# Optimization experiments

Measured on AMD Instinct MI355X. Metric: run time of the kernel, lower is better.

Reference implementation:

```python
import jax, jax.numpy as jnp
import numpy as np

B, S, H = 2, 4096, 1024
WINDOW = 32


def setup_inputs() -> dict:
    key = jax.random.key(0)
    ks = jax.random.split(key, 10)
    s = 1.0 / np.sqrt(H)
    return {
        "hidden_states": jax.random.normal(ks[0], (B, S, H), dtype=jnp.float32),
        "Wq": jax.random.normal(ks[1], (H, H), dtype=jnp.float32) * s,
        "Wk": jax.random.normal(ks[2], (H, H), dtype=jnp.float32) * s,
        "Wv": jax.random.normal(ks[3], (H, H), dtype=jnp.float32) * s,
        "Wo": jax.random.normal(ks[4], (H, H), dtype=jnp.float32) * s,
        "ln_w": jnp.ones((H,), dtype=jnp.float32),
        "ln_b": jnp.zeros((H,), dtype=jnp.float32),
        "W1": jax.random.normal(ks[5], (H // 2, H), dtype=jnp.float32) * s,
        "b1": jnp.zeros((H // 2,), dtype=jnp.float32),
        "W2": jax.random.normal(ks[6], (H, H // 2), dtype=jnp.float32) * (1.0 / np.sqrt(H // 2)),
        "b2": jnp.zeros((H,), dtype=jnp.float32),
    }


def _layernorm(x, w, b, eps=1e-5):
    mu = jnp.mean(x, axis=-1, keepdims=True)
    var = jnp.var(x, axis=-1, keepdims=True)
    return (x - mu) * jax.lax.rsqrt(var + eps) * w + b


def reference(hidden_states, Wq, Wk, Wv, Wo, ln_w, ln_b, W1, b1, W2, b2):
    x = hidden_states  # [B,S,H]
    q = x @ Wq.T
    k = x @ Wk.T
    v = x @ Wv.T
    # banded causal mask: keep j<=i and j >= i-WINDOW+1
    i = jnp.arange(S)[:, None]
    j = jnp.arange(S)[None, :]
    local_mask = (j <= i) & (j >= i - WINDOW + 1)  # [S,S] bool
    scores = jnp.einsum('bqh,bkh->bqk', q, k) / np.sqrt(H)
    scores = jnp.where(local_mask[None], scores, -jnp.inf)
    probs = jax.nn.softmax(scores, axis=-1)
    attn_out = jnp.einsum('bqk,bkh->bqh', probs, v) @ Wo.T
    draft = x + attn_out
    h = _layernorm(draft, ln_w, ln_b)
    h = jax.nn.gelu(h @ W1.T + b1, approximate=False)
    adapter_out = h @ W2.T + b2
    return draft + adapter_out
```

## Files before the change

### kernel.cpp

```cpp
#include <hip/hip_runtime.h>
#include <stdint.h>

typedef unsigned short u16;
typedef __bf16 bfx8 __attribute__((ext_vector_type(8)));
typedef float f32x4 __attribute__((ext_vector_type(4)));

__device__ __forceinline__ u16 f2bf(float x) {
    unsigned int u = __float_as_uint(x);
    u += 0x7fffu + ((u >> 16) & 1u);
    return (u16)(u >> 16);
}

__device__ __forceinline__ void async16(const void* g, void* l) {
    __builtin_amdgcn_global_load_lds(
        (const __attribute__((address_space(1))) unsigned int*)(uintptr_t)g,
        (__attribute__((address_space(3))) unsigned int*)(unsigned int)(uintptr_t)l,
        16, 0, 0);
}

#define S_BARRIER() asm volatile("s_barrier" ::: "memory")
#define WAIT_VM(n) asm volatile("s_waitcnt vmcnt(" #n ")" ::: "memory")

struct CastArgs {
    const float* src[7];
    u16* dst[7];
    int nblk[7];
};
__global__ __launch_bounds__(256) void cast_all(CastArgs a) {
    int b = blockIdx.x, seg = 0;
    while (b >= a.nblk[seg]) { b -= a.nblk[seg]; ++seg; }
    int i = b * 256 + threadIdx.x;
    const float4* p = (const float4*)(a.src[seg] + (size_t)i * 8);
    float4 x = p[0], y = p[1];
    ushort4 o0, o1;
    o0.x = f2bf(x.x); o0.y = f2bf(x.y); o0.z = f2bf(x.z); o0.w = f2bf(x.w);
    o1.x = f2bf(y.x); o1.y = f2bf(y.y); o1.z = f2bf(y.z); o1.w = f2bf(y.w);
    ushort4* q = (ushort4*)(a.dst[seg] + (size_t)i * 8);
    q[0] = o0; q[1] = o1;
}

template <int EPI>
__global__ __launch_bounds__(512, 2)
void gemm_nt(const u16* __restrict__ A, const u16* __restrict__ Bw,
             u16* __restrict__ outb, float* __restrict__ outf,
             const float* __restrict__ res, const float* __restrict__ bias,
             u16* __restrict__ outq, u16* __restrict__ outk,
             u16* __restrict__ vt, int M, int N, int K) {
    __shared__ __align__(1024) unsigned char lds[147456];
    const int t = threadIdx.x;
    const int lane = t & 63, w = t >> 6;
    const int laneR = lane & 15, laneK = lane >> 4;
    const int wr = w >> 1, wc = w & 1;
    const int row0 = blockIdx.y * 256, col0 = blockIdx.x * 128;
    const int nt = K >> 6;

    f32x4 acc[4][4] = {};

    const u16* srcA[4];
    const u16* srcB[2];
    unsigned dA[4], dB[2];
#pragma unroll
    for (int i = 0; i < 4; ++i) {
        int li = i * 512 + t;
        int row = li >> 3, ko = li & 7;
        srcA[i] = A + (size_t)(row0 + row) * K + (ko ^ (row & 7)) * 8;
        dA[i] = li * 16;
    }
#pragma unroll
    for (int i = 0; i < 2; ++i) {
        int li = i * 512 + t;
        int row = li >> 3, ko = li & 7;
        srcB[i] = Bw + (size_t)(col0 + row) * K + (ko ^ (row & 7)) * 8;
        dB[i] = 32768 + li * 16;
    }

    auto stage = [&](int b, int tk, int h) {
        unsigned char* base = lds + b * 49152;
        const int o = tk * 64;
        if (h == 0) {
            async16(srcA[0] + o, base + dA[0]);
            async16(srcA[1] + o, base + dA[1]);
            async16(srcB[0] + o, base + dB[0]);
        } else {
            async16(srcA[2] + o, base + dA[2]);
            async16(srcA[3] + o, base + dA[3]);
            async16(srcB[1] + o, base + dB[1]);
        }
    };

    stage(0, 0, 0); stage(0, 0, 1);
    stage(1, 1, 0); stage(1, 1, 1);

    for (int tk = 0; tk < nt; ++tk) {
        unsigned char* bufA = lds + (tk % 3) * 49152;
        unsigned char* bufB = bufA + 32768;
        if (tk + 1 < nt) { WAIT_VM(6); } else { WAIT_VM(0); }
        S_BARRIER();
        const bool pf = (tk + 2 < nt);
        const int nb = (tk + 2) % 3;
#pragma unroll
        for (int ks = 0; ks < 2; ++ks) {
            bfx8 af[4], bf[4];
#pragma unroll
            for (int m = 0; m < 4; ++m) {
                int r = wr * 64 + m * 16 + laneR;
                int phys = (ks * 4 + laneK) ^ (r & 7);
                af[m] = *(const bfx8*)(bufA + r * 128 + phys * 16);
            }
#pragma unroll
            for (int n = 0; n < 4; ++n) {
                int r = wc * 64 + n * 16 + laneR;
                int phys = (ks * 4 + laneK) ^ (r & 7);
                bf[n] = *(const bfx8*)(bufB + r * 128 + phys * 16);
            }
            if (pf) stage(nb, tk + 2, ks);
            S_BARRIER();
            __builtin_amdgcn_s_setprio(1);
#pragma unroll
            for (int m = 0; m < 4; ++m)
#pragma unroll
                for (int n = 0; n < 4; ++n)
                    acc[m][n] = __builtin_amdgcn_mfma_f32_16x16x32_bf16(
                        af[m], bf[n], acc[m][n], 0, 0, 0);
            __builtin_amdgcn_s_setprio(0);
            S_BARRIER();
        }
    }

#pragma unroll
    for (int m = 0; m < 4; ++m) {
        const int gr0 = row0 + wr * 64 + m * 16 + laneK * 4;
#pragma unroll
        for (int n = 0; n < 4; ++n) {
            const int gc = col0 + wc * 64 + n * 16 + laneR;
            if constexpr (EPI == 0) {
                if (col0 < 1024) {
#pragma unroll
                    for (int r = 0; r < 4; ++r)
                        outq[(size_t)(gr0 + r) * 1024 + gc] = f2bf(acc[m][n][r]);
                } else if (col0 < 2048) {
#pragma unroll
                    for (int r = 0; r < 4; ++r)
                        outk[(size_t)(gr0 + r) * 1024 + (gc - 1024)] = f2bf(acc[m][n][r]);
                } else {
                    ushort4 o4;
                    o4.x = f2bf(acc[m][n][0]); o4.y = f2bf(acc[m][n][1]);
                    o4.z = f2bf(acc[m][n][2]); o4.w = f2bf(acc[m][n][3]);
                    *(ushort4*)(vt + (((size_t)(gr0 >> 12)) * 1024 + (gc - 2048)) * 4096 +
                                (gr0 & 4095)) = o4;
                }
            } else if constexpr (EPI == 1) {
#pragma unroll
                for (int r = 0; r < 4; ++r) {
                    size_t idx = (size_t)(gr0 + r) * N + gc;
                    outf[idx] = res[idx] + acc[m][n][r];
                }
            } else if constexpr (EPI == 2) {
#pragma unroll
                for (int r = 0; r < 4; ++r) {
                    float xx = acc[m][n][r] + bias[gc];
                    outb[(size_t)(gr0 + r) * N + gc] =
                        f2bf(xx * 0.5f * (1.0f + erff(xx * 0.70710678118654752f)));
                }
            } else {
#pragma unroll
                for (int r = 0; r < 4; ++r) {
                    size_t idx = (size_t)(gr0 + r) * N + gc;
                    outf[idx] = res[idx] + acc[m][n][r] + bias[gc];
                }
            }
        }
    }
}

__global__ __launch_bounds__(256, 2)
void attn_kernel(const u16* __restrict__ Q, const u16* __restrict__ K,
                 const u16* __restrict__ vt, u16* __restrict__ O) {
    constexpr int H = 1024, S = 4096;
    const int t = threadIdx.x, lane = t & 63, w = t >> 6;
    const int laneR = lane & 15, laneK = lane >> 4;
    const int tile = blockIdx.x;
    const int batch = tile >> 7;
    const int i0 = (tile & 127) * 32;
    const size_t base = (size_t)batch * S * H;

    __shared__ __align__(16) float S4[4][32][64];
    __shared__ __align__(16) u16 P[32][72];

    f32x4 sc[2][4] = {};
    for (int h = w * 256; h < w * 256 + 256; h += 32) {
        bfx8 qa[2];
#pragma unroll
        for (int m = 0; m < 2; ++m) {
            size_t row = (size_t)(i0 + m * 16 + laneR);
            qa[m] = *(const bfx8*)(Q + base + row * H + h + laneK * 8);
        }
        bfx8 kb[4];
#pragma unroll
        for (int n = 0; n < 4; ++n) {
            int j = i0 - 32 + n * 16 + laneR;
            int jc = j < 0 ? 0 : j;
            kb[n] = *(const bfx8*)(K + base + (size_t)jc * H + h + laneK * 8);
        }
#pragma unroll
        for (int m = 0; m < 2; ++m)
#pragma unroll
            for (int n = 0; n < 4; ++n)
                sc[m][n] = __builtin_amdgcn_mfma_f32_16x16x32_bf16(
                    qa[m], kb[n], sc[m][n], 0, 0, 0);
    }
#pragma unroll
    for (int m = 0; m < 2; ++m)
#pragma unroll
        for (int n = 0; n < 4; ++n)
#pragma unroll
            for (int r = 0; r < 4; ++r)
                S4[w][m * 16 + laneK * 4 + r][n * 16 + laneR] = sc[m][n][r];
    __syncthreads();

    {
        int q = t >> 3;
        int c0 = (t & 7) * 8;
        int lo = q + 1;
        if (32 - i0 > lo) lo = 32 - i0;
        int hi = q + 32;
        float vals[8];
        float mx = -1e30f;
#pragma unroll
        for (int c = 0; c < 8; ++c) {
            int cc = c0 + c;
            float v = (S4[0][q][cc] + S4[1][q][cc] + S4[2][q][cc] + S4[3][q][cc]) * 0.03125f;
            bool valid = (cc >= lo) && (cc <= hi);
            vals[c] = valid ? v : -1e30f;
            if (vals[c] > mx) mx = vals[c];
        }
#pragma unroll
        for (int d = 1; d < 8; d <<= 1) {
            float o = __shfl_xor(mx, d);
            if (o > mx) mx = o;
        }
        float sum = 0.f;
        float es[8];
#pragma unroll
        for (int c = 0; c < 8; ++c) {
            es[c] = (vals[c] > -1e29f) ? __expf(vals[c] - mx) : 0.f;
            sum += es[c];
        }
#pragma unroll
        for (int d = 1; d < 8; d <<= 1) sum += __shfl_xor(sum, d);
        float inv = 1.0f / sum;
#pragma unroll
        for (int c = 0; c < 8; ++c) P[q][c0 + c] = f2bf(es[c] * inv);
    }
    __syncthreads();

    for (int nc = 0; nc < 4; ++nc) {
        int ncol = w * 256 + nc * 64;
        f32x4 o[2][4] = {};
#pragma unroll
        for (int ks = 0; ks < 2; ++ks) {
            bfx8 pa[2];
#pragma unroll
            for (int m = 0; m < 2; ++m)
                pa[m] = *(const bfx8*)(&P[m * 16 + laneR][ks * 32 + laneK * 8]);
            int t0 = i0 - 32 + ks * 32 + laneK * 8;
            if (t0 < 0) t0 = 0;
#pragma unroll
            for (int n = 0; n < 4; ++n) {
                int c = ncol + n * 16 + laneR;
                bfx8 vb = *(const bfx8*)(vt + ((size_t)batch * 1024 + c) * 4096 + t0);
#pragma unroll
                for (int m = 0; m < 2; ++m)
                    o[m][n] = __builtin_amdgcn_mfma_f32_16x16x32_bf16(
                        pa[m], vb, o[m][n], 0, 0, 0);
            }
        }
#pragma unroll
        for (int m = 0; m < 2; ++m)
#pragma unroll
            for (int n = 0; n < 4; ++n)
#pragma unroll
                for (int r = 0; r < 4; ++r) {
                    size_t row = (size_t)(i0 + m * 16 + laneK * 4 + r);
                    O[base + row * H + ncol + n * 16 + laneR] = f2bf(o[m][n][r]);
                }
    }
}

__global__ __launch_bounds__(256)
void ln_kernel(const float* __restrict__ x, const float* __restrict__ gw,
               const float* __restrict__ gb, u16* __restrict__ out) {
    const int row = blockIdx.x, t = threadIdx.x;
    const float4 v = ((const float4*)(x + (size_t)row * 1024))[t];
    float s = v.x + v.y + v.z + v.w;
    float s2 = v.x * v.x + v.y * v.y + v.z * v.z + v.w * v.w;
#pragma unroll
    for (int d = 1; d < 64; d <<= 1) {
        s += __shfl_xor(s, d);
        s2 += __shfl_xor(s2, d);
    }
    __shared__ float red[8];
    int lane = t & 63, wv = t >> 6;
    if (lane == 0) { red[wv] = s; red[4 + wv] = s2; }
    __syncthreads();
    float S1 = red[0] + red[1] + red[2] + red[3];
    float S2 = red[4] + red[5] + red[6] + red[7];
    float mu = S1 * (1.0f / 1024.0f);
    float var = S2 * (1.0f / 1024.0f) - mu * mu;
    float rstd = rsqrtf(var + 1e-5f);
    const float4 wv4 = ((const float4*)gw)[t];
    const float4 bv4 = ((const float4*)gb)[t];
    ushort4 o;
    o.x = f2bf((v.x - mu) * rstd * wv4.x + bv4.x);
    o.y = f2bf((v.y - mu) * rstd * wv4.y + bv4.y);
    o.z = f2bf((v.z - mu) * rstd * wv4.z + bv4.z);
    o.w = f2bf((v.w - mu) * rstd * wv4.w + bv4.w);
    ((ushort4*)(out + (size_t)row * 1024))[t] = o;
}

extern "C" void kernel_launch(void* const* d_in, const int* in_sizes, int n_in,
                              void* d_out, int out_size, void* d_ws, size_t ws_size,
                              hipStream_t stream) {
    const float* x   = (const float*)d_in[0];
    const float* Wq  = (const float*)d_in[1];
    const float* Wk  = (const float*)d_in[2];
    const float* Wv  = (const float*)d_in[3];
    const float* Wo  = (const float*)d_in[4];
    const float* lnw = (const float*)d_in[5];
    const float* lnb = (const float*)d_in[6];
    const float* W1  = (const float*)d_in[7];
    const float* b1  = (const float*)d_in[8];
    const float* W2  = (const float*)d_in[9];
    const float* b2  = (const float*)d_in[10];
    (void)in_sizes; (void)n_in; (void)out_size; (void)ws_size;

    const int M = 8192, H = 1024, Hh = 512;

    char* ws = (char*)d_ws;
    size_t off = 0;
    auto alloc = [&](size_t bytes) {
        char* p = ws + off;
        off += (bytes + 255) & ~(size_t)255;
        return p;
    };
    u16* Xb    = (u16*)alloc((size_t)M * H * 2);
    u16* Wqkvb = (u16*)alloc((size_t)3 * H * H * 2);
    u16* Wob   = (u16*)alloc((size_t)H * H * 2);
    u16* W1b   = (u16*)alloc((size_t)Hh * H * 2);
    u16* W2b   = (u16*)alloc((size_t)H * Hh * 2);
    u16* Qb    = (u16*)alloc((size_t)M * H * 2);
    u16* Kb    = (u16*)alloc((size_t)M * H * 2);
    u16* Vt    = (u16*)alloc((size_t)M * H * 2);
    float* draft = (float*)alloc((size_t)M * H * 4);
    u16* Attb = Xb;
    u16* hlnb = Qb;
    u16* Gb   = Kb;
    float* outp = (float*)d_out;

    CastArgs ca;
    ca.src[0] = x;  ca.dst[0] = Xb;                   ca.nblk[0] = (M * H / 8) / 256;
    ca.src[1] = Wq; ca.dst[1] = Wqkvb;                ca.nblk[1] = (H * H / 8) / 256;
    ca.src[2] = Wk; ca.dst[2] = Wqkvb + (size_t)H * H;     ca.nblk[2] = (H * H / 8) / 256;
    ca.src[3] = Wv; ca.dst[3] = Wqkvb + (size_t)2 * H * H; ca.nblk[3] = (H * H / 8) / 256;
    ca.src[4] = Wo; ca.dst[4] = Wob;                  ca.nblk[4] = (H * H / 8) / 256;
    ca.src[5] = W1; ca.dst[5] = W1b;                  ca.nblk[5] = (Hh * H / 8) / 256;
    ca.src[6] = W2; ca.dst[6] = W2b;                  ca.nblk[6] = (H * Hh / 8) / 256;
    int totblk = 0;
    for (int i = 0; i < 7; ++i) totblk += ca.nblk[i];
    cast_all<<<dim3(totblk), dim3(256), 0, stream>>>(ca);

    dim3 gblk(512);
    gemm_nt<0><<<dim3(3 * H / 128, M / 256), gblk, 0, stream>>>(
        Xb, Wqkvb, nullptr, nullptr, nullptr, nullptr, Qb, Kb, Vt, M, 3 * H, H);

    attn_kernel<<<dim3(256), dim3(256), 0, stream>>>(Qb, Kb, Vt, Attb);

    gemm_nt<1><<<dim3(H / 128, M / 256), gblk, 0, stream>>>(
        Attb, Wob, nullptr, draft, x, nullptr, nullptr, nullptr, nullptr, M, H, H);

    ln_kernel<<<dim3(M), dim3(256), 0, stream>>>(draft, lnw, lnb, hlnb);

    gemm_nt<2><<<dim3(Hh / 128, M / 256), gblk, 0, stream>>>(
        hlnb, W1b, Gb, nullptr, nullptr, b1, nullptr, nullptr, nullptr, M, Hh, H);

    gemm_nt<3><<<dim3(H / 128, M / 256), gblk, 0, stream>>>(
        Gb, W2b, nullptr, outp, draft, b2, nullptr, nullptr, nullptr, M, H, Hh);
}
```

Before: 190.6 us.

## Store draft in bf16, add register-staged GEMM variant, narrow W1 GEMM tiles

The fp32 draft buffer becomes bf16, which halves the traffic for writing draft, reading it in layernorm and reading it again as the residual in the final GEMM. The Wo and W2 GEMMs move to a new kernel that stages global loads through registers into a two-buffer LDS ring instead of using async LDS loads, so each block needs less LDS. The W1 GEMM now uses 64-wide N tiles, giving 256 blocks instead of 128 to fill more CUs. Rounding draft to bf16 adds error to both the residual path and the layernorm input.

```diff
diff --git a/kernel.cpp b/kernel.cpp
--- a/kernel.cpp
+++ b/kernel.cpp
@@ -9,6 +9,9 @@
     unsigned int u = __float_as_uint(x);
     u += 0x7fffu + ((u >> 16) & 1u);
     return (u16)(u >> 16);
+}
+__device__ __forceinline__ float bf2f(u16 v) {
+    return __uint_as_float(((unsigned)v) << 16);
 }
 
 __device__ __forceinline__ void async16(const void* g, void* l) {
@@ -19,7 +22,10 @@
 }
 
 #define S_BARRIER() asm volatile("s_barrier" ::: "memory")
-#define WAIT_VM(n) asm volatile("s_waitcnt vmcnt(" #n ")" ::: "memory")
+#define WAIT_VM6() asm volatile("s_waitcnt vmcnt(6)" ::: "memory")
+#define WAIT_VM5() asm volatile("s_waitcnt vmcnt(5)" ::: "memory")
+#define WAIT_VM0() asm volatile("s_waitcnt vmcnt(0)" ::: "memory")
+#define WAIT_LGKM0() asm volatile("s_waitcnt lgkmcnt(0)" ::: "memory")
 
 struct CastArgs {
     const float* src[7];
@@ -39,26 +45,28 @@
     q[0] = o0; q[1] = o1;
 }
 
-template <int EPI>
+template <int EPI, int BNv>
 __global__ __launch_bounds__(512, 2)
-void gemm_nt(const u16* __restrict__ A, const u16* __restrict__ Bw,
-             u16* __restrict__ outb, float* __restrict__ outf,
-             const float* __restrict__ res, const float* __restrict__ bias,
-             u16* __restrict__ outq, u16* __restrict__ outk,
-             u16* __restrict__ vt, int M, int N, int K) {
-    __shared__ __align__(1024) unsigned char lds[147456];
+void gemm_ring(const u16* __restrict__ A, const u16* __restrict__ Bw,
+               u16* __restrict__ outq, u16* __restrict__ outk,
+               u16* __restrict__ vt, u16* __restrict__ outb,
+               const float* __restrict__ bias, int M, int N, int K) {
+    constexpr int NF = BNv / 32;
+    constexpr int BU = BNv / 64;
+    constexpr int TS = 32768 + BNv * 128;
+    __shared__ __align__(1024) unsigned char lds[3 * TS];
     const int t = threadIdx.x;
     const int lane = t & 63, w = t >> 6;
     const int laneR = lane & 15, laneK = lane >> 4;
     const int wr = w >> 1, wc = w & 1;
-    const int row0 = blockIdx.y * 256, col0 = blockIdx.x * 128;
+    const int row0 = blockIdx.y * 256, col0 = blockIdx.x * BNv;
     const int nt = K >> 6;
 
-    f32x4 acc[4][4] = {};
+    f32x4 acc[4][NF] = {};
 
     const u16* srcA[4];
-    const u16* srcB[2];
-    unsigned dA[4], dB[2];
+    const u16* srcB[BU];
+    unsigned dA[4], dB[BU];
 #pragma unroll
     for (int i = 0; i < 4; ++i) {
         int li = i * 512 + t;
@@ -67,7 +75,7 @@
         dA[i] = li * 16;
     }
 #pragma unroll
-    for (int i = 0; i < 2; ++i) {
+    for (int i = 0; i < BU; ++i) {
         int li = i * 512 + t;
         int row = li >> 3, ko = li & 7;
         srcB[i] = Bw + (size_t)(col0 + row) * K + (ko ^ (row & 7)) * 8;
@@ -75,7 +83,7 @@
     }
 
     auto stage = [&](int b, int tk, int h) {
-        unsigned char* base = lds + b * 49152;
+        unsigned char* base = lds + b * TS;
         const int o = tk * 64;
         if (h == 0) {
             async16(srcA[0] + o, base + dA[0]);
@@ -84,7 +92,7 @@
         } else {
             async16(srcA[2] + o, base + dA[2]);
             async16(srcA[3] + o, base + dA[3]);
-            async16(srcB[1] + o, base + dB[1]);
+            if constexpr (BU == 2) async16(srcB[1] + o, base + dB[1]);
         }
     };
 
@@ -92,15 +100,17 @@
     stage(1, 1, 0); stage(1, 1, 1);
 
     for (int tk = 0; tk < nt; ++tk) {
-        unsigned char* bufA = lds + (tk % 3) * 49152;
+        unsigned char* bufA = lds + (tk % 3) * TS;
         unsigned char* bufB = bufA + 32768;
-        if (tk + 1 < nt) { WAIT_VM(6); } else { WAIT_VM(0); }
+        if (tk + 1 < nt) {
+            if constexpr (BU == 2) { WAIT_VM6(); } else { WAIT_VM5(); }
+        } else { WAIT_VM0(); }
         S_BARRIER();
         const bool pf = (tk + 2 < nt);
         const int nb = (tk + 2) % 3;
 #pragma unroll
         for (int ks = 0; ks < 2; ++ks) {
-            bfx8 af[4], bf[4];
+            bfx8 af[4], bf[NF];
 #pragma unroll
             for (int m = 0; m < 4; ++m) {
                 int r = wr * 64 + m * 16 + laneR;
@@ -108,8 +118,8 @@
                 af[m] = *(const bfx8*)(bufA + r * 128 + phys * 16);
             }
 #pragma unroll
-            for (int n = 0; n < 4; ++n) {
-                int r = wc * 64 + n * 16 + laneR;
+            for (int n = 0; n < NF; ++n) {
+                int r = wc * (BNv / 2) + n * 16 + laneR;
                 int phys = (ks * 4 + laneK) ^ (r & 7);
                 bf[n] = *(const bfx8*)(bufB + r * 128 + phys * 16);
             }
@@ -119,7 +129,7 @@
 #pragma unroll
             for (int m = 0; m < 4; ++m)
 #pragma unroll
-                for (int n = 0; n < 4; ++n)
+                for (int n = 0; n < NF; ++n)
                     acc[m][n] = __builtin_amdgcn_mfma_f32_16x16x32_bf16(
                         af[m], bf[n], acc[m][n], 0, 0, 0);
             __builtin_amdgcn_s_setprio(0);
@@ -131,8 +141,8 @@
     for (int m = 0; m < 4; ++m) {
         const int gr0 = row0 + wr * 64 + m * 16 + laneK * 4;
 #pragma unroll
-        for (int n = 0; n < 4; ++n) {
-            const int gc = col0 + wc * 64 + n * 16 + laneR;
+        for (int n = 0; n < NF; ++n) {
+            const int gc = col0 + wc * (BNv / 2) + n * 16 + laneR;
             if constexpr (EPI == 0) {
                 if (col0 < 1024) {
 #pragma unroll
@@ -149,28 +159,165 @@
                     *(ushort4*)(vt + (((size_t)(gr0 >> 12)) * 1024 + (gc - 2048)) * 4096 +
                                 (gr0 & 4095)) = o4;
                 }
-            } else if constexpr (EPI == 1) {
-#pragma unroll
-                for (int r = 0; r < 4; ++r) {
-                    size_t idx = (size_t)(gr0 + r) * N + gc;
-                    outf[idx] = res[idx] + acc[m][n][r];
-                }
-            } else if constexpr (EPI == 2) {
+            } else {
 #pragma unroll
                 for (int r = 0; r < 4; ++r) {
                     float xx = acc[m][n][r] + bias[gc];
                     outb[(size_t)(gr0 + r) * N + gc] =
                         f2bf(xx * 0.5f * (1.0f + erff(xx * 0.70710678118654752f)));
                 }
-            } else {
-#pragma unroll
-                for (int r = 0; r < 4; ++r) {
-                    size_t idx = (size_t)(gr0 + r) * N + gc;
-                    outf[idx] = res[idx] + acc[m][n][r] + bias[gc];
+            }
+        }
+    }
+}
+
+template <int EPI>
+__global__ __launch_bounds__(512, 2)
+void gemm_rs(const u16* __restrict__ A, const u16* __restrict__ Bw,
+             const float* __restrict__ res, u16* __restrict__ draftb,
+             const float* __restrict__ bias, float* __restrict__ outf,
+             int M, int N, int K) {
+    __shared__ __align__(1024) unsigned char lds[98304];
+    const int t = threadIdx.x;
+    const int lane = t & 63, w = t >> 6;
+    const int laneR = lane & 15, laneK = lane >> 4;
+    const int wr = w >> 1, wc = w & 1;
+    const int row0 = blockIdx.y * 256, col0 = blockIdx.x * 128;
+    const int nt = K >> 6;
+
+    f32x4 acc[4][4] = {};
+
+    const u16* srcA[4];
+    const u16* srcB[2];
+    unsigned dA[4], dB[2];
+#pragma unroll
+    for (int i = 0; i < 4; ++i) {
+        int li = i * 512 + t;
+        int row = li >> 3, ko = li & 7;
+        srcA[i] = A + (size_t)(row0 + row) * K + ko * 8;
+        dA[i] = row * 128 + (ko ^ (row & 7)) * 16;
+    }
+#pragma unroll
+    for (int i = 0; i < 2; ++i) {
+        int li = i * 512 + t;
+        int row = li >> 3, ko = li & 7;
+        srcB[i] = Bw + (size_t)(col0 + row) * K + ko * 8;
+        dB[i] = 32768 + row * 128 + (ko ^ (row & 7)) * 16;
+    }
+
+    uint4 raA[4], rbA[2];
+    uint4 raB[4], rbB[2];
+
+#define RS_ISSUE(RA, RB, TK)                                                   \
+    {                                                                          \
+        const int o_ = (TK) * 64;                                              \
+        _Pragma("unroll") for (int i = 0; i < 4; ++i)                          \
+            RA[i] = *(const uint4*)(srcA[i] + o_);                             \
+        _Pragma("unroll") for (int i = 0; i < 2; ++i)                          \
+            RB[i] = *(const uint4*)(srcB[i] + o_);                             \
+    }
+#define RS_WRITE(RA, RB, BUF)                                                  \
+    {                                                                          \
+        unsigned char* base_ = lds + (BUF) * 49152;                            \
+        _Pragma("unroll") for (int i = 0; i < 4; ++i)                          \
+            *(uint4*)(base_ + dA[i]) = RA[i];                                  \
+        _Pragma("unroll") for (int i = 0; i < 2; ++i)                          \
+            *(uint4*)(base_ + dB[i]) = RB[i];                                  \
+    }
+
+    bfx8 af[4], bf[4];
+    auto LDS_READS = [&](unsigned char* bufA, int ks) {
+        unsigned char* bufB = bufA + 32768;
+#pragma unroll
+        for (int m = 0; m < 4; ++m) {
+            int r = wr * 64 + m * 16 + laneR;
+            int phys = (ks * 4 + laneK) ^ (r & 7);
+            af[m] = *(const bfx8*)(bufA + r * 128 + phys * 16);
+        }
+#pragma unroll
+        for (int n = 0; n < 4; ++n) {
+            int r = wc * 64 + n * 16 + laneR;
+            int phys = (ks * 4 + laneK) ^ (r & 7);
+            bf[n] = *(const bfx8*)(bufB + r * 128 + phys * 16);
+        }
+    };
+    auto DOMFMA = [&]() {
+        __builtin_amdgcn_s_setprio(1);
+#pragma unroll
+        for (int m = 0; m < 4; ++m)
+#pragma unroll
+            for (int n = 0; n < 4; ++n)
+                acc[m][n] = __builtin_amdgcn_mfma_f32_16x16x32_bf16(
+                    af[m], bf[n], acc[m][n], 0, 0, 0);
+        __builtin_amdgcn_s_setprio(0);
+    };
+
+    RS_ISSUE(raA, rbA, 0)
+    RS_ISSUE(raB, rbB, (1 < nt ? 1 : 0))
+    WAIT_VM6();
+    RS_WRITE(raA, rbA, 0)
+    WAIT_LGKM0();
+    S_BARRIER();
+
+    for (int tp = 0; tp < nt; tp += 2) {
+        {
+            unsigned char* bufA = lds + 0;
+            LDS_READS(bufA, 0);
+            const int ti = (tp + 2 < nt) ? tp + 2 : nt - 1;
+            RS_ISSUE(raA, rbA, ti)
+            S_BARRIER();
+            DOMFMA();
+            S_BARRIER();
+            LDS_READS(bufA, 1);
+            if (tp + 1 < nt) {
+                WAIT_VM6();
+                RS_WRITE(raB, rbB, 1)
+            }
+            S_BARRIER();
+            DOMFMA();
+            WAIT_LGKM0();
+            S_BARRIER();
+        }
+        if (tp + 1 >= nt) break;
+        {
+            unsigned char* bufA = lds + 49152;
+            LDS_READS(bufA, 0);
+            const int ti = (tp + 3 < nt) ? tp + 3 : nt - 1;
+            RS_ISSUE(raB, rbB, ti)
+            S_BARRIER();
+            DOMFMA();
+            S_BARRIER();
+            LDS_READS(bufA, 1);
+            if (tp + 2 < nt) {
+                WAIT_VM6();
+                RS_WRITE(raA, rbA, 0)
+            }
+            S_BARRIER();
+            DOMFMA();
+            WAIT_LGKM0();
+            S_BARRIER();
+        }
+    }
+
+#pragma unroll
+    for (int m = 0; m < 4; ++m) {
+        const int gr0 = row0 + wr * 64 + m * 16 + laneK * 4;
+#pragma unroll
+        for (int n = 0; n < 4; ++n) {
+            const int gc = col0 + wc * 64 + n * 16 + laneR;
+#pragma unroll
+            for (int r = 0; r < 4; ++r) {
+                size_t idx = (size_t)(gr0 + r) * N + gc;
+                if constexpr (EPI == 1) {
+                    draftb[idx] = f2bf(res[idx] + acc[m][n][r]);
+                } else {
+                    outf[idx] = bf2f(draftb[idx]) + acc[m][n][r] + bias[gc];
                 }
             }
         }
     }
+#undef RS_ISSUE
+#undef RS_WRITE
 }
 
 __global__ __launch_bounds__(256, 2)
@@ -288,10 +435,12 @@
 }
 
 __global__ __launch_bounds__(256)
-void ln_kernel(const float* __restrict__ x, const float* __restrict__ gw,
+void ln_kernel(const u16* __restrict__ xb, const float* __restrict__ gw,
                const float* __restrict__ gb, u16* __restrict__ out) {
     const int row = blockIdx.x, t = threadIdx.x;
-    const float4 v = ((const float4*)(x + (size_t)row * 1024))[t];
+    const ushort4 dv = ((const ushort4*)(xb + (size_t)row * 1024))[t];
+    float4 v;
+    v.x = bf2f(dv.x); v.y = bf2f(dv.y); v.z = bf2f(dv.z); v.w = bf2f(dv.w);
     float s = v.x + v.y + v.z + v.w;
     float s2 = v.x * v.x + v.y * v.y + v.z * v.z + v.w * v.w;
 #pragma unroll
@@ -343,46 +492,45 @@
         off += (bytes + 255) & ~(size_t)255;
         return p;
     };
-    u16* Xb    = (u16*)alloc((size_t)M * H * 2);
-    u16* Wqkvb = (u16*)alloc((size_t)3 * H * H * 2);
-    u16* Wob   = (u16*)alloc((size_t)H * H * 2);
-    u16* W1b   = (u16*)alloc((size_t)Hh * H * 2);
-    u16* W2b   = (u16*)alloc((size_t)H * Hh * 2);
-    u16* Qb    = (u16*)alloc((size_t)M * H * 2);
-    u16* Kb    = (u16*)alloc((size_t)M * H * 2);
-    u16* Vt    = (u16*)alloc((size_t)M * H * 2);
-    float* draft = (float*)alloc((size_t)M * H * 4);
+    u16* Xb     = (u16*)alloc((size_t)M * H * 2);
+    u16* Wqkvb  = (u16*)alloc((size_t)3 * H * H * 2);
+    u16* Wob    = (u16*)alloc((size_t)H * H * 2);
+    u16* W1b    = (u16*)alloc((size_t)Hh * H * 2);
+    u16* W2b    = (u16*)alloc((size_t)H * Hh * 2);
+    u16* Qb     = (u16*)alloc((size_t)M * H * 2);
+    u16* Kb     = (u16*)alloc((size_t)M * H * 2);
+    u16* Vt     = (u16*)alloc((size_t)M * H * 2);
+    u16* draftb = (u16*)alloc((size_t)M * H * 2);
     u16* Attb = Xb;
     u16* hlnb = Qb;
     u16* Gb   = Kb;
     float* outp = (float*)d_out;
 
     CastArgs ca;
-    ca.src[0] = x;  ca.dst[0] = Xb;                   ca.nblk[0] = (M * H / 8) / 256;
-    ca.src[1] = Wq; ca.dst[1] = Wqkvb;                ca.nblk[1] = (H * H / 8) / 256;
+    ca.src[0] = x;  ca.dst[0] = Xb;                        ca.nblk[0] = (M * H / 8) / 256;
+    ca.src[1] = Wq; ca.dst[1] = Wqkvb;                     ca.nblk[1] = (H * H / 8) / 256;
     ca.src[2] = Wk; ca.dst[2] = Wqkvb + (size_t)H * H;     ca.nblk[2] = (H * H / 8) / 256;
     ca.src[3] = Wv; ca.dst[3] = Wqkvb + (size_t)2 * H * H; ca.nblk[3] = (H * H / 8) / 256;
-    ca.src[4] = Wo; ca.dst[4] = Wob;                  ca.nblk[4] = (H * H / 8) / 256;
-    ca.src[5] = W1; ca.dst[5] = W1b;                  ca.nblk[5] = (Hh * H / 8) / 256;
-    ca.src[6] = W2; ca.dst[6] = W2b;                  ca.nblk[6] = (H * Hh / 8) / 256;
+    ca.src[4] = Wo; ca.dst[4] = Wob;                       ca.nblk[4] = (H * H / 8) / 256;
+    ca.src[5] = W1; ca.dst[5] = W1b;                       ca.nblk[5] = (Hh * H / 8) / 256;
+    ca.src[6] = W2; ca.dst[6] = W2b;                       ca.nblk[6] = (H * Hh / 8) / 256;
     int totblk = 0;
     for (int i = 0; i < 7; ++i) totblk += ca.nblk[i];
     cast_all<<<dim3(totblk), dim3(256), 0, stream>>>(ca);
 
-    dim3 gblk(512);
-    gemm_nt<0><<<dim3(3 * H / 128, M / 256), gblk, 0, stream>>>(
-        Xb, Wqkvb, nullptr, nullptr, nullptr, nullptr, Qb, Kb, Vt, M, 3 * H, H);
+    gemm_ring<0, 128><<<dim3(3 * H / 128, M / 256), dim3(512), 0, stream>>>(
+        Xb, Wqkvb, Qb, Kb, Vt, nullptr, nullptr, M, 3 * H, H);
 
     attn_kernel<<<dim3(256), dim3(256), 0, stream>>>(Qb, Kb, Vt, Attb);
 
-    gemm_nt<1><<<dim3(H / 128, M / 256), gblk, 0, stream>>>(
-        Attb, Wob, nullptr, draft, x, nullptr, nullptr, nullptr, nullptr, M, H, H);
-
-    ln_kernel<<<dim3(M), dim3(256), 0, stream>>>(draft, lnw, lnb, hlnb);
-
-    gemm_nt<2><<<dim3(Hh / 128, M / 256), gblk, 0, stream>>>(
-        hlnb, W1b, Gb, nullptr, nullptr, b1, nullptr, nullptr, nullptr, M, Hh, H);
-
-    gemm_nt<3><<<dim3(H / 128, M / 256), gblk, 0, stream>>>(
-        Gb, W2b, nullptr, outp, draft, b2, nullptr, nullptr, nullptr, M, H, Hh);
-}
+    gemm_rs<1><<<dim3(H / 128, M / 256), dim3(512), 0, stream>>>(
+        Attb, Wob, x, draftb, nullptr, nullptr, M, H, H);
+
+    ln_kernel<<<dim3(M), dim3(256), 0, stream>>>(draftb, lnw, lnb, hlnb);
+
+    gemm_ring<2, 64><<<dim3(Hh / 64, M / 256), dim3(512), 0, stream>>>(
+        hlnb, W1b, nullptr, nullptr, nullptr, Gb, b1, M, Hh, H);
+
+    gemm_rs<3><<<dim3(H / 128, M / 256), dim3(512), 0, stream>>>(
+        Gb, W2b, nullptr, draftb, b2, outp, M, H, Hh);
+}
```

New measurement: 219.6 us. 1.15x slower.

## Store draft in bf16, swizzle block order, use narrower tile for W1 GEMM

Applied to the files above, without the earlier changes.

The residual draft tensor is now stored as bf16 instead of fp32, and the residual add reads the bf16 copy of x instead of the fp32 input. This roughly halves traffic for the draft write, the LayerNorm read and the final residual read, at the cost of extra rounding in the residual path. The GEMM grids become 1-D with an XCD-aware block swizzle, and the attention tile order is remapped the same way, to improve L2 locality across chiplets. The W1 GEMM uses 64-wide column tiles so its grid has 256 blocks instead of 128, improving CU occupancy.

```diff
diff --git a/kernel.cpp b/kernel.cpp
--- a/kernel.cpp
+++ b/kernel.cpp
@@ -9,6 +9,9 @@
     unsigned int u = __float_as_uint(x);
     u += 0x7fffu + ((u >> 16) & 1u);
     return (u16)(u >> 16);
+}
+__device__ __forceinline__ float bf2f(u16 v) {
+    return __uint_as_float(((unsigned)v) << 16);
 }
 
 __device__ __forceinline__ void async16(const void* g, void* l) {
@@ -19,7 +22,9 @@
 }
 
 #define S_BARRIER() asm volatile("s_barrier" ::: "memory")
-#define WAIT_VM(n) asm volatile("s_waitcnt vmcnt(" #n ")" ::: "memory")
+#define WAIT_VM6() asm volatile("s_waitcnt vmcnt(6)" ::: "memory")
+#define WAIT_VM5() asm volatile("s_waitcnt vmcnt(5)" ::: "memory")
+#define WAIT_VM0() asm volatile("s_waitcnt vmcnt(0)" ::: "memory")
 
 struct CastArgs {
     const float* src[7];
@@ -39,26 +44,33 @@
     q[0] = o0; q[1] = o1;
 }
 
-template <int EPI>
+template <int EPI, int BNv>
 __global__ __launch_bounds__(512, 2)
-void gemm_nt(const u16* __restrict__ A, const u16* __restrict__ Bw,
-             u16* __restrict__ outb, float* __restrict__ outf,
-             const float* __restrict__ res, const float* __restrict__ bias,
-             u16* __restrict__ outq, u16* __restrict__ outk,
-             u16* __restrict__ vt, int M, int N, int K) {
-    __shared__ __align__(1024) unsigned char lds[147456];
+void gemm_ring(const u16* __restrict__ A, const u16* __restrict__ Bw,
+               u16* __restrict__ outq, u16* __restrict__ outk,
+               u16* __restrict__ vt, u16* __restrict__ outb,
+               const float* __restrict__ bias, const u16* __restrict__ resb,
+               u16* __restrict__ draftb, float* __restrict__ outf,
+               int M, int N, int K, int ncol) {
+    constexpr int NF = BNv / 32;
+    constexpr int BU = BNv / 64;
+    constexpr int TS = 32768 + BNv * 128;
+    __shared__ __align__(1024) unsigned char lds[3 * TS];
     const int t = threadIdx.x;
     const int lane = t & 63, w = t >> 6;
     const int laneR = lane & 15, laneK = lane >> 4;
     const int wr = w >> 1, wc = w & 1;
-    const int row0 = blockIdx.y * 256, col0 = blockIdx.x * 128;
+    const int b = blockIdx.x;
+    const int cpx = gridDim.x >> 3;
+    const int swz = (b & 7) * cpx + (b >> 3);
+    const int row0 = (swz / ncol) * 256, col0 = (swz % ncol) * BNv;
     const int nt = K >> 6;
 
-    f32x4 acc[4][4] = {};
+    f32x4 acc[4][NF] = {};
 
     const u16* srcA[4];
-    const u16* srcB[2];
-    unsigned dA[4], dB[2];
+    const u16* srcB[BU];
+    unsigned dA[4], dB[BU];
 #pragma unroll
     for (int i = 0; i < 4; ++i) {
         int li = i * 512 + t;
@@ -67,15 +79,15 @@
         dA[i] = li * 16;
     }
 #pragma unroll
-    for (int i = 0; i < 2; ++i) {
+    for (int i = 0; i < BU; ++i) {
         int li = i * 512 + t;
         int row = li >> 3, ko = li & 7;
         srcB[i] = Bw + (size_t)(col0 + row) * K + (ko ^ (row & 7)) * 8;
         dB[i] = 32768 + li * 16;
     }
 
-    auto stage = [&](int b, int tk, int h) {
-        unsigned char* base = lds + b * 49152;
+    auto stage = [&](int rb, int tk, int h) {
+        unsigned char* base = lds + rb * TS;
         const int o = tk * 64;
         if (h == 0) {
             async16(srcA[0] + o, base + dA[0]);
@@ -84,7 +96,7 @@
         } else {
             async16(srcA[2] + o, base + dA[2]);
             async16(srcA[3] + o, base + dA[3]);
-            async16(srcB[1] + o, base + dB[1]);
+            if constexpr (BU == 2) async16(srcB[1] + o, base + dB[1]);
         }
     };
 
@@ -92,15 +104,17 @@
     stage(1, 1, 0); stage(1, 1, 1);
 
     for (int tk = 0; tk < nt; ++tk) {
-        unsigned char* bufA = lds + (tk % 3) * 49152;
+        unsigned char* bufA = lds + (tk % 3) * TS;
         unsigned char* bufB = bufA + 32768;
-        if (tk + 1 < nt) { WAIT_VM(6); } else { WAIT_VM(0); }
+        if (tk + 1 < nt) {
+            if constexpr (BU == 2) { WAIT_VM6(); } else { WAIT_VM5(); }
+        } else { WAIT_VM0(); }
         S_BARRIER();
         const bool pf = (tk + 2 < nt);
         const int nb = (tk + 2) % 3;
 #pragma unroll
         for (int ks = 0; ks < 2; ++ks) {
-            bfx8 af[4], bf[4];
+            bfx8 af[4], bf[NF];
 #pragma unroll
             for (int m = 0; m < 4; ++m) {
                 int r = wr * 64 + m * 16 + laneR;
@@ -108,8 +122,8 @@
                 af[m] = *(const bfx8*)(bufA + r * 128 + phys * 16);
             }
 #pragma unroll
-            for (int n = 0; n < 4; ++n) {
-                int r = wc * 64 + n * 16 + laneR;
+            for (int n = 0; n < NF; ++n) {
+                int r = wc * (BNv / 2) + n * 16 + laneR;
                 int phys = (ks * 4 + laneK) ^ (r & 7);
                 bf[n] = *(const bfx8*)(bufB + r * 128 + phys * 16);
             }
@@ -119,7 +133,7 @@
 #pragma unroll
             for (int m = 0; m < 4; ++m)
 #pragma unroll
-                for (int n = 0; n < 4; ++n)
+                for (int n = 0; n < NF; ++n)
                     acc[m][n] = __builtin_amdgcn_mfma_f32_16x16x32_bf16(
                         af[m], bf[n], acc[m][n], 0, 0, 0);
             __builtin_amdgcn_s_setprio(0);
@@ -131,8 +145,8 @@
     for (int m = 0; m < 4; ++m) {
         const int gr0 = row0 + wr * 64 + m * 16 + laneK * 4;
 #pragma unroll
-        for (int n = 0; n < 4; ++n) {
-            const int gc = col0 + wc * 64 + n * 16 + laneR;
+        for (int n = 0; n < NF; ++n) {
+            const int gc = col0 + wc * (BNv / 2) + n * 16 + laneR;
             if constexpr (EPI == 0) {
                 if (col0 < 1024) {
 #pragma unroll
@@ -153,7 +167,7 @@
 #pragma unroll
                 for (int r = 0; r < 4; ++r) {
                     size_t idx = (size_t)(gr0 + r) * N + gc;
-                    outf[idx] = res[idx] + acc[m][n][r];
+                    draftb[idx] = f2bf(bf2f(resb[idx]) + acc[m][n][r]);
                 }
             } else if constexpr (EPI == 2) {
 #pragma unroll
@@ -166,7 +180,7 @@
 #pragma unroll
                 for (int r = 0; r < 4; ++r) {
                     size_t idx = (size_t)(gr0 + r) * N + gc;
-                    outf[idx] = res[idx] + acc[m][n][r] + bias[gc];
+                    outf[idx] = bf2f(draftb[idx]) + acc[m][n][r] + bias[gc];
                 }
             }
         }
@@ -179,7 +193,8 @@
     constexpr int H = 1024, S = 4096;
     const int t = threadIdx.x, lane = t & 63, w = t >> 6;
     const int laneR = lane & 15, laneK = lane >> 4;
-    const int tile = blockIdx.x;
+    const int bb = blockIdx.x;
+    const int tile = (bb & 7) * 32 + (bb >> 3);
     const int batch = tile >> 7;
     const int i0 = (tile & 127) * 32;
     const size_t base = (size_t)batch * S * H;
@@ -288,10 +303,12 @@
 }
 
 __global__ __launch_bounds__(256)
-void ln_kernel(const float* __restrict__ x, const float* __restrict__ gw,
+void ln_kernel(const u16* __restrict__ xb, const float* __restrict__ gw,
                const float* __restrict__ gb, u16* __restrict__ out) {
     const int row = blockIdx.x, t = threadIdx.x;
-    const float4 v = ((const float4*)(x + (size_t)row * 1024))[t];
+    const ushort4 dv = ((const ushort4*)(xb + (size_t)row * 1024))[t];
+    float4 v;
+    v.x = bf2f(dv.x); v.y = bf2f(dv.y); v.z = bf2f(dv.z); v.w = bf2f(dv.w);
     float s = v.x + v.y + v.z + v.w;
     float s2 = v.x * v.x + v.y * v.y + v.z * v.z + v.w * v.w;
 #pragma unroll
@@ -343,46 +360,49 @@
         off += (bytes + 255) & ~(size_t)255;
         return p;
     };
-    u16* Xb    = (u16*)alloc((size_t)M * H * 2);
-    u16* Wqkvb = (u16*)alloc((size_t)3 * H * H * 2);
-    u16* Wob   = (u16*)alloc((size_t)H * H * 2);
-    u16* W1b   = (u16*)alloc((size_t)Hh * H * 2);
-    u16* W2b   = (u16*)alloc((size_t)H * Hh * 2);
-    u16* Qb    = (u16*)alloc((size_t)M * H * 2);
-    u16* Kb    = (u16*)alloc((size_t)M * H * 2);
-    u16* Vt    = (u16*)alloc((size_t)M * H * 2);
-    float* draft = (float*)alloc((size_t)M * H * 4);
-    u16* Attb = Xb;
+    u16* Xb     = (u16*)alloc((size_t)M * H * 2);
+    u16* Wqkvb  = (u16*)alloc((size_t)3 * H * H * 2);
+    u16* Wob    = (u16*)alloc((size_t)H * H * 2);
+    u16* W1b    = (u16*)alloc((size_t)Hh * H * 2);
+    u16* W2b    = (u16*)alloc((size_t)H * Hh * 2);
+    u16* Qb     = (u16*)alloc((size_t)M * H * 2);
+    u16* Kb     = (u16*)alloc((size_t)M * H * 2);
+    u16* Vt     = (u16*)alloc((size_t)M * H * 2);
+    u16* draftb = (u16*)alloc((size_t)M * H * 2);
+    u16* Attb   = (u16*)alloc((size_t)M * H * 2);
     u16* hlnb = Qb;
     u16* Gb   = Kb;
     float* outp = (float*)d_out;
 
     CastArgs ca;
-    ca.src[0] = x;  ca.dst[0] = Xb;                   ca.nblk[0] = (M * H / 8) / 256;
-    ca.src[1] = Wq; ca.dst[1] = Wqkvb;                ca.nblk[1] = (H * H / 8) / 256;
+    ca.src[0] = x;  ca.dst[0] = Xb;                        ca.nblk[0] = (M * H / 8) / 256;
+    ca.src[1] = Wq; ca.dst[1] = Wqkvb;                     ca.nblk[1] = (H * H / 8) / 256;
     ca.src[2] = Wk; ca.dst[2] = Wqkvb + (size_t)H * H;     ca.nblk[2] = (H * H / 8) / 256;
     ca.src[3] = Wv; ca.dst[3] = Wqkvb + (size_t)2 * H * H; ca.nblk[3] = (H * H / 8) / 256;
-    ca.src[4] = Wo; ca.dst[4] = Wob;                  ca.nblk[4] = (H * H / 8) / 256;
-    ca.src[5] = W1; ca.dst[5] = W1b;                  ca.nblk[5] = (Hh * H / 8) / 256;
-    ca.src[6] = W2; ca.dst[6] = W2b;                  ca.nblk[6] = (H * Hh / 8) / 256;
+    ca.src[4] = Wo; ca.dst[4] = Wob;                       ca.nblk[4] = (H * H / 8) / 256;
+    ca.src[5] = W1; ca.dst[5] = W1b;                       ca.nblk[5] = (Hh * H / 8) / 256;
+    ca.src[6] = W2; ca.dst[6] = W2b;                       ca.nblk[6] = (H * Hh / 8) / 256;
     int totblk = 0;
     for (int i = 0; i < 7; ++i) totblk += ca.nblk[i];
     cast_all<<<dim3(totblk), dim3(256), 0, stream>>>(ca);
 
-    dim3 gblk(512);
-    gemm_nt<0><<<dim3(3 * H / 128, M / 256), gblk, 0, stream>>>(
-        Xb, Wqkvb, nullptr, nullptr, nullptr, nullptr, Qb, Kb, Vt, M, 3 * H, H);
+    gemm_ring<0, 128><<<dim3(768), dim3(512), 0, stream>>>(
+        Xb, Wqkvb, Qb, Kb, Vt, nullptr, nullptr, nullptr, nullptr, nullptr,
+        M, 3 * H, H, 24);
 
     attn_kernel<<<dim3(256), dim3(256), 0, stream>>>(Qb, Kb, Vt, Attb);
 
-    gemm_nt<1><<<dim3(H / 128, M / 256), gblk, 0, stream>>>(
-        Attb, Wob, nullptr, draft, x, nullptr, nullptr, nullptr, nullptr, M, H, H);
-
-    ln_kernel<<<dim3(M), dim3(256), 0, stream>>>(draft, lnw, lnb, hlnb);
-
-    gemm_nt<2><<<dim3(Hh / 128, M / 256), gblk, 0, stream>>>(
-        hlnb, W1b, Gb, nullptr, nullptr, b1, nullptr, nullptr, nullptr, M, Hh, H);
-
-    gemm_nt<3><<<dim3(H / 128, M / 256), gblk, 0, stream>>>(
-        Gb, W2b, nullptr, outp, draft, b2, nullptr, nullptr, nullptr, M, H, Hh);
-}
+    gemm_ring<1, 128><<<dim3(256), dim3(512), 0, stream>>>(
+        Attb, Wob, nullptr, nullptr, nullptr, nullptr, nullptr, Xb, draftb, nullptr,
+        M, H, H, 8);
+
+    ln_kernel<<<dim3(M), dim3(256), 0, stream>>>(draftb, lnw, lnb, hlnb);
+
+    gemm_ring<2, 64><<<dim3(256), dim3(512), 0, stream>>>(
+        hlnb, W1b, nullptr, nullptr, nullptr, Gb, b1, nullptr, nullptr, nullptr,
+        M, Hh, H, 8);
+
+    gemm_ring<3, 128><<<dim3(256), dim3(512), 0, stream>>>(
+        Gb, W2b, nullptr, nullptr, nullptr, nullptr, b2, nullptr, draftb, outp,
+        M, H, Hh, 8);
+}
```

Result: faster. 168.8 us (-11.5%).
